# Kernel tuning notes

Hardware: AMD Instinct MI355X
Metric: run time of the kernel (lower is better)

## Reference

```python
import jax, jax.numpy as jnp
import numpy as np

# Layered-DAG regularization of the dynamic active_path graph.
H, N, BATCH, D, R = 6, 16, 32, 512, 64   # hop levels, nodes/level, batch, dim, low-rank
M = (H - 1) * N                           # nodes with weights (levels 1..H-1)
ETA_W = 0.015
LAM_C, LAM_R = 0.65, 0.35
THETA0 = 0.5
SPEC_MIN, SPEC_MAX = 0.3, 4.0
BETA1, BETA2, EPS = 0.9, 0.999, 1e-8
W_MAX = float(np.sqrt(D) * 2.0)
DW_CLIP = 5.0


def _spectral_norm(A1, B1):
    # largest singular value of W = A1 @ B1.T via power iteration using only low-rank products
    d = A1.shape[0]
    def body(_, u):
        w = A1 @ (B1.T @ (B1 @ (A1.T @ u)))  # (W W^T) u
        return w / (jnp.linalg.norm(w) + 1e-12)
    u0 = jnp.ones((d,), A1.dtype) / jnp.sqrt(jnp.asarray(d, A1.dtype))
    u = jax.lax.fori_loop(0, 20, body, u0)
    return jnp.linalg.norm(B1 @ (A1.T @ u))


def _update_node(A1, B1, mA, vA, mB, vB, Vin, T_local):
    # dual-signal (contrastive + retrograde) weight update, Adam step t=1, is_positive=True
    W = A1 @ B1.T                       # (D, D)
    Vw = Vin @ W.T                      # (BATCH, D) pre-activation (record.V_weighted)
    Vout = jnp.tanh(Vw)                 # record.V_out (tanh primitive)
    fprime = 1.0 - Vout ** 2            # primitive_derivative for tanh
    goodness = (Vout ** 2).sum(-1).mean()
    theta = THETA0 * ((Vin ** 2).sum(-1).mean() + 1e-9)   # goodness_scale_input=True
    delta = goodness - theta
    Vout_grad = (Vout * fprime * delta).mean(0)
    Vin_mean = Vin.mean(0)
    dW_c = jnp.outer(Vout_grad, Vin_mean)
    dW_r = jnp.outer(T_local.mean(0) * fprime.mean(0), Vin_mean)
    dW = LAM_C * dW_c + LAM_R * dW_r
    gnorm = jnp.linalg.norm(dW)
    dW = dW * jnp.where(gnorm > DW_CLIP, DW_CLIP / (gnorm + 1e-12), 1.0)
    gA = dW @ B1
    gB = dW.T @ A1
    mA_n = BETA1 * mA + (1 - BETA1) * gA
    vA_n = BETA2 * vA + (1 - BETA2) * gA ** 2
    A_new = A1 - ETA_W * (mA_n / (1 - BETA1)) / (jnp.sqrt(vA_n / (1 - BETA2)) + EPS)
    mB_n = BETA1 * mB + (1 - BETA1) * gB
    vB_n = BETA2 * vB + (1 - BETA2) * gB ** 2
    B_new = B1 - ETA_W * (mB_n / (1 - BETA1)) / (jnp.sqrt(vB_n / (1 - BETA2)) + EPS)
    return jnp.clip(A_new, -W_MAX, W_MAX), jnp.clip(B_new, -W_MAX, W_MAX)


def _forward(Y_hat, Y_star, V_edges, A, Bw, m_A, v_A, m_B, v_B):
    T_v = (Y_star - Y_hat) / jnp.sqrt(jnp.asarray(D, Y_hat.dtype))
    mse = jnp.mean((Y_star - Y_hat) ** 2)

    # proportional blame: per-edge mean-over-batch L2 norm of the contribution
    norms = jnp.linalg.norm(V_edges, axis=-1).mean(-1)           # (H-1, Ndst, Nsrc)
    w_blame = norms / (norms.sum(-1, keepdims=True) + 1e-9)

    spec = jax.vmap(jax.vmap(_spectral_norm))(A, Bw)             # (H-1, N)
    scale = jax.lax.stop_gradient(jnp.clip(spec, SPEC_MIN, SPEC_MAX))  # torch.tensor() detaches

    # retrograde flow in reverse topological (hop) order; output node = (level H-1, node 0)
    T_top = jnp.zeros((N, BATCH, D), Y_hat.dtype).at[0].set(T_v)

    def step(T_curr, xs):
        w_h, s_h = xs                                            # (Ndst,Nsrc), (Ndst,)
        tnorm = jnp.linalg.norm(T_curr, axis=-1).mean(-1)        # (Ndst,)
        edge_t = s_h[:, None] * w_h * tnorm[:, None]             # ||T_upstream|| per edge
        T_prev = jnp.einsum('j,ji,jbd->ibd', s_h, w_h, T_curr)   # blame-weighted scatter
        return T_prev, (T_prev, edge_t)

    _, (Ts, edge_t) = jax.lax.scan(step, T_top, (w_blame[::-1], scale[::-1]))
    T_all = jnp.concatenate([Ts[::-1], T_top[None]], axis=0)     # (H, N, BATCH, D), by level
    edge_tensions = edge_t[::-1]                                 # (H-1, Ndst, Nsrc)

    V_in = V_edges.sum(axis=2)                                   # inbox sum -> (H-1, N, BATCH, D)
    T_upd = T_all[1:]                                            # tensions at non-input nodes

    sh = (M, D, R)
    A_new, B_new = jax.vmap(_update_node)(
        A.reshape(sh), Bw.reshape(sh), m_A.reshape(sh), v_A.reshape(sh),
        m_B.reshape(sh), v_B.reshape(sh),
        V_in.reshape(M, BATCH, D), T_upd.reshape(M, BATCH, D))
    return (mse, edge_tensions,
            A_new.reshape(H - 1, N, D, R), B_new.reshape(H - 1, N, D, R), T_all)


def setup_inputs():
    key = jax.random.key(0)
    k = jax.random.split(key, 7)
    sd = 1.0 / np.sqrt(D)
    return {
        "Y_hat": jax.random.normal(k[0], (BATCH, D), jnp.float32),
        "Y_star": jax.random.normal(k[1], (BATCH, D), jnp.float32),
        "V_edges": jax.random.normal(k[2], (H - 1, N, N, BATCH, D), jnp.float32),
        "A": jax.random.normal(k[3], (H - 1, N, D, R), jnp.float32) * sd,
        "Bw": jax.random.normal(k[4], (H - 1, N, D, R), jnp.float32) * sd,
        "m_A": jnp.zeros((H - 1, N, D, R), jnp.float32),
        "v_A": jax.random.uniform(k[5], (H - 1, N, D, R), jnp.float32) * 1e-4,
        "m_B": jnp.zeros((H - 1, N, D, R), jnp.float32),
        "v_B": jax.random.uniform(k[6], (H - 1, N, D, R), jnp.float32) * 1e-4,
    }


def reference(Y_hat, Y_star, V_edges, A, Bw, m_A, v_A, m_B, v_B):
    return _forward(Y_hat, Y_star, V_edges, A, Bw, m_A, v_A, m_B, v_B)
```

## Files before the change

### kernel.cpp

```cpp
#include <hip/hip_runtime.h>
#include <math.h>

#define DEV static __device__ __forceinline__

constexpr int NB    = 16;
constexpr int BATCH = 32;
constexpr int DDIM  = 512;
constexpr int RK    = 64;
constexpr int LAY   = 5;
constexpr int MM    = 80;
constexpr int TLS   = NB * BATCH * DDIM;

constexpr float ETA_W   = 0.015f;
constexpr float LAM_C   = 0.65f, LAM_R = 0.35f;
constexpr float THETA0  = 0.5f;
constexpr float SPEC_MIN = 0.3f, SPEC_MAX = 4.0f;
constexpr float DW_CLIP = 5.0f;
constexpr float W_MAX   = 45.254833995939045f;
constexpr float RSQ_D   = 0.044194173824159216f;

constexpr int OUT_MSE  = 0;
constexpr int OUT_EDGE = 1;
constexpr int OUT_A    = 1281;
constexpr int OUT_B    = OUT_A + MM * DDIM * RK;
constexpr int OUT_T    = OUT_B + MM * DDIM * RK;

constexpr int SCR_GP   = 1284;
constexpr int SCR_VIN  = SCR_GP + 2621440;

constexpr int WS_NORMB  = 0;
constexpr int WS_TVN    = 40960;
constexpr int WS_TVM    = 41000;
constexpr int WS_COEF   = 41600;
constexpr int WS_SCALE  = 41700;
constexpr int WS_Y0P    = 41800;
constexpr int WS_VM     = 62300;
constexpr int WS_P      = 103300;
constexpr int WS_Q      = 108450;
constexpr int WS_GC     = 113600;

DEV float wave_reduce(float v) {
  #pragma unroll
  for (int o = 32; o > 0; o >>= 1) v += __shfl_down(v, o, 64);
  return v;
}

DEV float block_reduce_512(float v, float* sred) {
  v = wave_reduce(v);
  __syncthreads();
  if ((threadIdx.x & 63) == 0) sred[threadIdx.x >> 6] = v;
  __syncthreads();
  float s = 0.f;
  #pragma unroll
  for (int k = 0; k < 8; ++k) s += sred[k];
  return s;
}

DEV float bcast_lane(float v, int lane) {
  return __int_as_float(__builtin_amdgcn_readlane(__float_as_int(v), lane));
}

__global__ __launch_bounds__(256) void k_stage1(const float* __restrict__ V,
    const float* __restrict__ yh, const float* __restrict__ ys,
    const float* __restrict__ Aw, const float* __restrict__ Bww,
    float* __restrict__ out, float* __restrict__ ws) {
  __shared__ float smem[8448];
  int bid = blockIdx.x, t = threadIdx.x;
  if (bid < 2560) {
    float* nbuf = smem;
    float* vbuf = smem + 2048;
    int b = bid & 31, j = (bid >> 5) & 15, hh = bid >> 9;
    const float* base = V + (size_t)(((hh*16 + j)*16)*32 + b) * 512;
    int g = t >> 7, u = t & 127;
    float vx = 0.f, vy = 0.f, vz = 0.f, vw = 0.f;
    #pragma unroll
    for (int io = 0; io < 8; ++io) {
      int i = io * 2 + g;
      float4 v = ((const float4*)(base + (size_t)i * 16384))[u];
      nbuf[i * 128 + u] = v.x*v.x + v.y*v.y + v.z*v.z + v.w*v.w;
      vx += v.x; vy += v.y; vz += v.z; vw += v.w;
    }
    vbuf[g * 512 + u * 4 + 0] = vx;
    vbuf[g * 512 + u * 4 + 1] = vy;
    vbuf[g * 512 + u * 4 + 2] = vz;
    vbuf[g * 512 + u * 4 + 3] = vw;
    __syncthreads();
    {
      float2 o;
      o.x = vbuf[2 * t]     + vbuf[512 + 2 * t];
      o.y = vbuf[2 * t + 1] + vbuf[512 + 2 * t + 1];
      ((float2*)(out + SCR_VIN + (size_t)((hh*16 + j)*32 + b) * 512))[t] = o;
    }
    int w = t >> 6, lane = t & 63;
    #pragma unroll
    for (int k = 0; k < 4; ++k) {
      int i = w * 4 + k;
      float s = nbuf[i * 128 + lane] + nbuf[i * 128 + lane + 64];
      s = wave_reduce(s);
      if (lane == 0)
        ws[WS_NORMB + (size_t)b * 1280 + (hh*16 + j) * 16 + i] = sqrtf(s);
    }
  } else if (bid < 2592) {
    int b = bid - 2560;
    float2 a = ((const float2*)(yh + (size_t)b * 512))[t];
    float2 c = ((const float2*)(ys + (size_t)b * 512))[t];
    float d0 = c.x - a.x, d1 = c.y - a.y;
    float s = d0*d0 + d1*d1;
    s = wave_reduce(s);
    if ((t & 63) == 0) smem[t >> 6] = s;
    __syncthreads();
    if (t == 0)
      ws[WS_TVN + b] = sqrtf(smem[0]+smem[1]+smem[2]+smem[3]) * RSQ_D;
  } else if (bid == 2592) {
    float s = 0.f;
    for (int i = t; i < 4096; i += 256) {
      float4 a = ((const float4*)yh)[i], b = ((const float4*)ys)[i];
      float d0 = b.x-a.x, d1 = b.y-a.y, d2 = b.z-a.z, d3 = b.w-a.w;
      s += d0*d0 + d1*d1 + d2*d2 + d3*d3;
    }
    s = wave_reduce(s);
    if ((t & 63) == 0) smem[t >> 6] = s;
    __syncthreads();
    if (t == 0)
      out[OUT_MSE] = (smem[0]+smem[1]+smem[2]+smem[3]) * (1.f/16384.f);
  } else if (bid == 2593) {
    float s0 = 0.f, s1 = 0.f;
    #pragma unroll 4
    for (int b = 0; b < 32; ++b) {
      s0 += ys[b*512 + t]       - yh[b*512 + t];
      s1 += ys[b*512 + t + 256] - yh[b*512 + t + 256];
    }
    ws[WS_TVM + t]       = s0 * (RSQ_D / 32.f);
    ws[WS_TVM + t + 256] = s1 * (RSQ_D / 32.f);
  } else {
    float* tile = smem;
    float (*y0s)[64] = (float(*)[64])(smem + 8192);
    int bid0 = bid - 2594;
    int slice = bid0 & 3, side = (bid0 >> 2) & 1, m = bid0 >> 3;
    const float* src = (side ? Bww : Aw) + (size_t)m * 32768 + slice * 8192;
    #pragma unroll
    for (int k = 0; k < 8; ++k)
      ((float4*)tile)[t + k * 256] = ((const float4*)src)[t + k * 256];
    __syncthreads();
    {
      int r = t & 63, q = t >> 6;
      float s = 0.f;
      #pragma unroll 8
      for (int dd = q * 32; dd < q * 32 + 32; ++dd) s += tile[dd * 64 + r];
      y0s[q][r] = s;
    }
    __syncthreads();
    if (side == 0 && t < 64)
      ws[WS_Y0P + (m * 4 + slice) * 64 + t] = y0s[0][t] + y0s[1][t] + y0s[2][t] + y0s[3][t];
    float acc[4][4];
    #pragma unroll
    for (int i = 0; i < 4; ++i)
      #pragma unroll
      for (int k = 0; k < 4; ++k) acc[i][k] = 0.f;
    int r1 = (t >> 4) * 4, r2 = (t & 15) * 4;
    #pragma unroll 4
    for (int dd = 0; dd < 128; ++dd) {
      float4 a1 = *(const float4*)&tile[dd * 64 + r1];
      float4 a2 = *(const float4*)&tile[dd * 64 + r2];
      float av[4] = {a1.x, a1.y, a1.z, a1.w};
      float bv[4] = {a2.x, a2.y, a2.z, a2.w};
      #pragma unroll
      for (int i = 0; i < 4; ++i)
        #pragma unroll
        for (int k = 0; k < 4; ++k) acc[i][k] += av[i] * bv[k];
    }
    float* outp = out + SCR_GP + (size_t)((m * 2 + side) * 4 + slice) * 4096;
    #pragma unroll
    for (int i = 0; i < 4; ++i) {
      float4 v; v.x = acc[i][0]; v.y = acc[i][1]; v.z = acc[i][2]; v.w = acc[i][3];
      *(float4*)&outp[(r1 + i) * 64 + r2] = v;
    }
  }
}

__global__ __launch_bounds__(64, 1) void k_power(const float* __restrict__ out,
                                                 float* __restrict__ ws) {
  int m = blockIdx.x;
  int r = threadIdx.x;
  const float* gp = out + SCR_GP + (size_t)(m * 2 + 0) * 16384;
  const float* hp = out + SCR_GP + (size_t)(m * 2 + 1) * 16384;
  float Gc[64], Hc[64];
  #pragma unroll
  for (int c4 = 0; c4 < 16; ++c4) {
    const float* gb = gp + r * 64 + c4 * 4;
    float4 g0 = *(const float4*)(gb);
    float4 g1 = *(const float4*)(gb + 4096);
    float4 g2 = *(const float4*)(gb + 8192);
    float4 g3 = *(const float4*)(gb + 12288);
    Gc[c4*4+0] = g0.x+g1.x+g2.x+g3.x;
    Gc[c4*4+1] = g0.y+g1.y+g2.y+g3.y;
    Gc[c4*4+2] = g0.z+g1.z+g2.z+g3.z;
    Gc[c4*4+3] = g0.w+g1.w+g2.w+g3.w;
    const float* hb = hp + r * 64 + c4 * 4;
    float4 h0 = *(const float4*)(hb);
    float4 h1 = *(const float4*)(hb + 4096);
    float4 h2 = *(const float4*)(hb + 8192);
    float4 h3 = *(const float4*)(hb + 12288);
    Hc[c4*4+0] = h0.x+h1.x+h2.x+h3.x;
    Hc[c4*4+1] = h0.y+h1.y+h2.y+h3.y;
    Hc[c4*4+2] = h0.z+h1.z+h2.z+h3.z;
    Hc[c4*4+3] = h0.w+h1.w+h2.w+h3.w;
  }
  float y = (ws[WS_Y0P + (m*4+0)*64 + r] + ws[WS_Y0P + (m*4+1)*64 + r] +
             ws[WS_Y0P + (m*4+2)*64 + r] + ws[WS_Y0P + (m*4+3)*64 + r]) * RSQ_D;
  for (int it = 0; it < 20; ++it) {
    float z0 = 0.f, z1 = 0.f, z2 = 0.f, z3 = 0.f;
    #pragma unroll
    for (int c = 0; c < 16; ++c) {
      z0 = fmaf(Hc[c],      bcast_lane(y, c),      z0);
      z1 = fmaf(Hc[c + 16], bcast_lane(y, c + 16), z1);
      z2 = fmaf(Hc[c + 32], bcast_lane(y, c + 32), z2);
      z3 = fmaf(Hc[c + 48], bcast_lane(y, c + 48), z3);
    }
    float z = (z0 + z1) + (z2 + z3);
    float t0 = 0.f, t1 = 0.f, t2 = 0.f, t3 = 0.f;
    #pragma unroll
    for (int c = 0; c < 16; ++c) {
      t0 = fmaf(Gc[c],      bcast_lane(z, c),      t0);
      t1 = fmaf(Gc[c + 16], bcast_lane(z, c + 16), t1);
      t2 = fmaf(Gc[c + 32], bcast_lane(z, c + 32), t2);
      t3 = fmaf(Gc[c + 48], bcast_lane(z, c + 48), t3);
    }
    float tt = (t0 + t1) + (t2 + t3);
    float zt = z * tt;
    #pragma unroll
    for (int o = 32; o > 0; o >>= 1) zt += __shfl_xor(zt, o, 64);
    y = tt / (sqrtf(zt) + 1e-12f);
  }
  float z0 = 0.f, z1 = 0.f, z2 = 0.f, z3 = 0.f;
  #pragma unroll
  for (int c = 0; c < 16; ++c) {
    z0 = fmaf(Hc[c],      bcast_lane(y, c),      z0);
    z1 = fmaf(Hc[c + 16], bcast_lane(y, c + 16), z1);
    z2 = fmaf(Hc[c + 32], bcast_lane(y, c + 32), z2);
    z3 = fmaf(Hc[c + 48], bcast_lane(y, c + 48), z3);
  }
  float z = (z0 + z1) + (z2 + z3);
  float yz = y * z;
  #pragma unroll
  for (int o = 32; o > 0; o >>= 1) yz += __shfl_xor(yz, o, 64);
  if (r == 0)
    ws[WS_SCALE + m] = fminf(fmaxf(sqrtf(yz), SPEC_MIN), SPEC_MAX);
}

constexpr int MTP = 516;
constexpr int YVP = 36;

__global__ __launch_bounds__(512) void k_node(const float* __restrict__ Aw,
    const float* __restrict__ Bww, float* __restrict__ out, float* __restrict__ ws) {
  __shared__ float MT[64 * MTP];
  __shared__ float R2[4096];
  __shared__ float gcol[512];
  __shared__ float sred[8];
  __shared__ float coefs[96];
  int m = blockIdx.x;
  int t = threadIdx.x;
  const float* A1  = Aw  + (size_t)m * 32768;
  const float* B1  = Bww + (size_t)m * 32768;
  const float* Vin = out + SCR_VIN + (size_t)m * 16384;
  int hh = m >> 4, j = m & 15;

  if (t < 256) {
    #pragma unroll
    for (int h = 0; h < 5; ++h) {
      float n = 0.f;
      #pragma unroll 8
      for (int b = 0; b < 32; ++b)
        n += ws[WS_NORMB + (size_t)b * 1280 + h * 256 + t];
      n *= (1.f / 32.f);
      float s = n;
      s += __shfl_xor(s, 1, 64);
      s += __shfl_xor(s, 2, 64);
      s += __shfl_xor(s, 4, 64);
      s += __shfl_xor(s, 8, 64);
      R2[h * 256 + t] = ws[WS_SCALE + h * 16 + (t >> 4)] * n / (s + 1e-9f);
    }
    if (t < 16) coefs[80 + t] = (t == 0) ? 1.f : 0.f;
  }
  __syncthreads();
  if (t < 16) {
    for (int h = 4; h >= 0; --h) {
      float s = 0.f;
      #pragma unroll
      for (int jj = 0; jj < 16; ++jj)
        s += R2[h * 256 + jj * 16 + t] * coefs[(h + 1) * 16 + jj];
      coefs[h * 16 + t] = s;
    }
  }
  __syncthreads();
  if (m == 0) {
    if (t < 256) {
      float tvs = 0.f;
      #pragma unroll
      for (int b = 0; b < 32; ++b) tvs += ws[WS_TVN + b];
      float tvmean = tvs * (1.f / 32.f);
      #pragma unroll
      for (int h = 0; h < 5; ++h)
        out[OUT_EDGE + h * 256 + t] = R2[h * 256 + t] * coefs[(h + 1) * 16 + (t >> 4)] * tvmean;
    }
    if (t < 96) ws[WS_COEF + t] = coefs[t];
  }
  float coefval = coefs[(hh + 1) * 16 + j];

  auto stageT = [&](const float* src) {
    #pragma unroll
    for (int ch = 0; ch < 16; ++ch) {
      int g = ch * 2048 + t * 4;
      int d = g >> 6, r = g & 63;
      float4 v = *(const float4*)(src + g);
      MT[(r+0)*MTP + d] = v.x;
      MT[(r+1)*MTP + d] = v.y;
      MT[(r+2)*MTP + d] = v.z;
      MT[(r+3)*MTP + d] = v.w;
    }
  };

  stageT(B1);
  __syncthreads();

  {
    int rl = t & 31, bq = t >> 5;
    int b0 = bq * 2;
    float a00 = 0.f, a01 = 0.f, a10 = 0.f, a11 = 0.f;
    const float4* vp0 = (const float4*)(Vin + (size_t)b0 * 512);
    const float4* vp1 = (const float4*)(Vin + (size_t)(b0 + 1) * 512);
    #pragma unroll 4
    for (int d4 = 0; d4 < 128; ++d4) {
      float4 m0 = *(const float4*)&MT[rl * MTP + d4 * 4];
      float4 m1 = *(const float4*)&MT[(rl + 32) * MTP + d4 * 4];
      float4 v0 = vp0[d4];
      float4 v1 = vp1[d4];
      a00 += m0.x*v0.x + m0.y*v0.y + m0.z*v0.z + m0.w*v0.w;
      a01 += m0.x*v1.x + m0.y*v1.y + m0.z*v1.z + m0.w*v1.w;
      a10 += m1.x*v0.x + m1.y*v0.y + m1.z*v0.z + m1.w*v0.w;
      a11 += m1.x*v1.x + m1.y*v1.y + m1.z*v1.z + m1.w*v1.w;
    }
    R2[rl * YVP + b0]            = a00;
    R2[rl * YVP + b0 + 1]        = a01;
    R2[(rl + 32) * YVP + b0]     = a10;
    R2[(rl + 32) * YVP + b0 + 1] = a11;
  }
  __syncthreads();
  if (t < 64) {
    float s = 0.f;
    #pragma unroll 8
    for (int b = 0; b < 32; ++b) s += R2[t * YVP + b];
    ws[WS_P + m * 64 + t] = s * (1.f / 32.f);
  }
  float tmean, ssin, ssvm;
  {
    int d = t;
    float sv = 0.f, sq = 0.f;
    #pragma unroll 4
    for (int b = 0; b < 32; ++b) {
      float v = Vin[b * 512 + d];
      sv += v; sq += v * v;
    }
    float vmean = sv * (1.f / 32.f);
    tmean = coefval * ws[WS_TVM + d];
    ws[WS_VM + m * 512 + d] = vmean;
    ssin = block_reduce_512(sq, sred) * (1.f / 32.f);
    ssvm = block_reduce_512(vmean * vmean, sred);
  }
  __syncthreads();
  stageT(A1);
  __syncthreads();
  float gs = 0.f;
  float vga[4] = {0.f, 0.f, 0.f, 0.f}, fpa[4] = {0.f, 0.f, 0.f, 0.f};
  {
    int d4 = t >> 2, bg = t & 3;
    float acc[4][8];
    #pragma unroll
    for (int i = 0; i < 4; ++i)
      #pragma unroll
      for (int k = 0; k < 8; ++k) acc[i][k] = 0.f;
    #pragma unroll 2
    for (int rr = 0; rr < 64; ++rr) {
      float4 at = *(const float4*)&MT[rr * MTP + d4 * 4];
      float4 ya = *(const float4*)&R2[rr * YVP + bg * 8];
      float4 yb = *(const float4*)&R2[rr * YVP + bg * 8 + 4];
      float av[4] = {at.x, at.y, at.z, at.w};
      float yv[8] = {ya.x, ya.y, ya.z, ya.w, yb.x, yb.y, yb.z, yb.w};
      #pragma unroll
      for (int i = 0; i < 4; ++i)
        #pragma unroll
        for (int k = 0; k < 8; ++k) acc[i][k] += av[i] * yv[k];
    }
    #pragma unroll
    for (int i = 0; i < 4; ++i)
      #pragma unroll
      for (int k = 0; k < 8; ++k) {
        float vw = acc[i][k];
        float x = fminf(fmaxf(vw * 2.f, -40.f), 40.f);
        float e = __expf(x);
        float vo = (e - 1.f) / (e + 1.f);
        float fp = 1.f - vo * vo;
        gs += vo * vo;
        vga[i] += vo * fp;
        fpa[i] += fp;
      }
  }
  __syncthreads();
  {
    int d4 = t >> 2, bg = t & 3;
    #pragma unroll
    for (int i = 0; i < 4; ++i) {
      R2[bg * 512 + d4 * 4 + i] = vga[i];
      R2[2048 + bg * 512 + d4 * 4 + i] = fpa[i];
    }
  }
  float goodness = block_reduce_512(gs, sred) * (1.f / 32.f);
  float delta = goodness - THETA0 * (ssin + 1e-9f);
  {
    int d = t;
    float vg = R2[d] + R2[512 + d] + R2[1024 + d] + R2[1536 + d];
    float fp = R2[2048 + d] + R2[2048 + 512 + d] + R2[2048 + 1024 + d] + R2[2048 + 1536 + d];
    float g = LAM_C * delta * vg * (1.f / 32.f) + LAM_R * tmean * (fp * (1.f / 32.f));
    float gn2 = block_reduce_512(g * g, sred);
    float gnorm = sqrtf(gn2) * sqrtf(ssvm);
    float clipf = gnorm > DW_CLIP ? DW_CLIP / (gnorm + 1e-12f) : 1.f;
    float gcv = g * clipf;
    ws[WS_GC + m * 512 + d] = gcv;
    gcol[d] = gcv;
  }
  __syncthreads();
  {
    int r = t & 63, dq = t >> 6;
    float s = 0.f;
    #pragma unroll
    for (int k = 0; k < 16; ++k) {
      int d = dq * 64 + k * 4;
      float4 at = *(const float4*)&MT[r * MTP + d];
      float4 gv = *(const float4*)&gcol[d];
      s += at.x*gv.x + at.y*gv.y + at.z*gv.z + at.w*gv.w;
    }
    R2[dq * 64 + r] = s;
  }
  __syncthreads();
  if (t < 64) {
    float s = 0.f;
    #pragma unroll
    for (int p8 = 0; p8 < 8; ++p8) s += R2[p8 * 64 + t];
    ws[WS_Q + m * 64 + t] = s;
  }
}

constexpr int TW_BLOCKS = 1536;
constexpr int AD_HALF4  = 655360;

__global__ __launch_bounds__(256) void k_final(const float* __restrict__ yh,
    const float* __restrict__ ys,
    const float* __restrict__ Aw, const float* __restrict__ Bww,
    const float* __restrict__ mA, const float* __restrict__ vA,
    const float* __restrict__ mB, const float* __restrict__ vB,
    const float* __restrict__ ws, float* __restrict__ out) {
  int bid = blockIdx.x, t = threadIdx.x;
  if (bid < TW_BLOCKS) {
    int g0 = (bid * 256 + t) * 4;
    int li = g0 >> 14;
    int bd = g0 & 16383;
    float4 a = *(const float4*)(yh + bd);
    float4 b = *(const float4*)(ys + bd);
    float cf = ws[WS_COEF + li] * RSQ_D;
    out[OUT_T + g0 + 0] = cf * (b.x - a.x);
    out[OUT_T + g0 + 1] = cf * (b.y - a.y);
    out[OUT_T + g0 + 2] = cf * (b.z - a.z);
    out[OUT_T + g0 + 3] = cf * (b.w - a.w);
    return;
  }
  int idx = (bid - TW_BLOCKS) * 256 + t;
  bool isB = idx >= AD_HALF4;
  int e = (isB ? idx - AD_HALF4 : idx) * 4;
  int m = e >> 15;
  int rem = e & 32767;
  int d = rem >> 6;
  int r = rem & 63;
  float4 g4;
  const float *w0, *m0, *v0;
  int obase;
  if (!isB) {
    float gc = ws[WS_GC + m * 512 + d];
    float4 p = *(const float4*)&ws[WS_P + m * 64 + r];
    g4.x = gc * p.x; g4.y = gc * p.y; g4.z = gc * p.z; g4.w = gc * p.w;
    w0 = Aw; m0 = mA; v0 = vA; obase = OUT_A;
  } else {
    float vm = ws[WS_VM + m * 512 + d];
    float4 q = *(const float4*)&ws[WS_Q + m * 64 + r];
    g4.x = vm * q.x; g4.y = vm * q.y; g4.z = vm * q.z; g4.w = vm * q.w;
    w0 = Bww; m0 = mB; v0 = vB; obase = OUT_B;
  }
  float4 a4 = *(const float4*)&w0[e];
  float4 mm4 = *(const float4*)&m0[e];
  float4 vv4 = *(const float4*)&v0[e];
  float ga[4] = {g4.x, g4.y, g4.z, g4.w};
  float aa[4] = {a4.x, a4.y, a4.z, a4.w};
  float ma[4] = {mm4.x, mm4.y, mm4.z, mm4.w};
  float va[4] = {vv4.x, vv4.y, vv4.z, vv4.w};
  #pragma unroll
  for (int i = 0; i < 4; ++i) {
    float g = ga[i];
    float mn = 0.9f * ma[i] + 0.1f * g;
    float vn = 0.999f * va[i] + 0.001f * g * g;
    float u = aa[i] - ETA_W * (mn * 10.f) / (sqrtf(vn * 1000.f) + 1e-8f);
    u = fminf(fmaxf(u, -W_MAX), W_MAX);
    out[obase + e + i] = u;
  }
}

extern "C" void kernel_launch(void* const* d_in, const int* in_sizes, int n_in,
                              void* d_out, int out_size, void* d_ws, size_t ws_size,
                              hipStream_t stream) {
  (void)in_sizes; (void)n_in; (void)out_size; (void)ws_size;
  const float* Yh = (const float*)d_in[0];
  const float* Ys = (const float*)d_in[1];
  const float* V  = (const float*)d_in[2];
  const float* Aw = (const float*)d_in[3];
  const float* Bw = (const float*)d_in[4];
  const float* mA = (const float*)d_in[5];
  const float* vA = (const float*)d_in[6];
  const float* mB = (const float*)d_in[7];
  const float* vB = (const float*)d_in[8];
  float* out = (float*)d_out;
  float* ws  = (float*)d_ws;

  k_stage1<<<2594 + 640, 256, 0, stream>>>(V, Yh, Ys, Aw, Bw, out, ws);
  k_power<<<80, 64, 0, stream>>>(out, ws);
  k_node<<<80, 512, 0, stream>>>(Aw, Bw, out, ws);
  k_final<<<TW_BLOCKS + 2 * (AD_HALF4 / 256), 256, 0, stream>>>(
      Yh, Ys, Aw, Bw, mA, vA, mB, vB, ws, out);
}
```

Baseline: 116.3 us.

## Split per-node kernel into Yv GEMV kernel and Vw kernel using pre-transposed A

Moves the B^T·Vin product out of the 80-block node kernel into a separate 160-block kernel, and has stage1 write a transposed copy of A into scratch so the node kernel reads A^T from global memory instead of staging it transposed in a large LDS buffer. The stage1 tile is padded to reduce bank conflicts. The intent is to cut the large per-block LDS footprint and the serial staging work in the low-occupancy node kernel. In exchange it adds a kernel launch, extra global writes and reads of the transposed A, and uncached global reads inside the inner GEMM loop.

```diff
diff --git a/kernel.cpp b/kernel.cpp
--- a/kernel.cpp
+++ b/kernel.cpp
@@ -26,7 +26,9 @@
 constexpr int OUT_T    = OUT_B + MM * DDIM * RK;
 
 constexpr int SCR_GP   = 1284;
-constexpr int SCR_VIN  = SCR_GP + 2621440;
+constexpr int SCR_YV   = 1284;
+constexpr int SCR_AT   = 2622724;
+constexpr int SCR_VIN  = 5244164;
 
 constexpr int WS_NORMB  = 0;
 constexpr int WS_TVN    = 40960;
@@ -60,11 +62,13 @@
   return __int_as_float(__builtin_amdgcn_readlane(__float_as_int(v), lane));
 }
 
+constexpr int GTP = 68;
+
 __global__ __launch_bounds__(256) void k_stage1(const float* __restrict__ V,
     const float* __restrict__ yh, const float* __restrict__ ys,
     const float* __restrict__ Aw, const float* __restrict__ Bww,
     float* __restrict__ out, float* __restrict__ ws) {
-  __shared__ float smem[8448];
+  __shared__ float smem[128 * GTP + 256];
   int bid = blockIdx.x, t = threadIdx.x;
   if (bid < 2560) {
     float* nbuf = smem;
@@ -134,24 +138,40 @@
     ws[WS_TVM + t + 256] = s1 * (RSQ_D / 32.f);
   } else {
     float* tile = smem;
-    float (*y0s)[64] = (float(*)[64])(smem + 8192);
+    float (*y0s)[64] = (float(*)[64])(smem + 128 * GTP);
     int bid0 = bid - 2594;
     int slice = bid0 & 3, side = (bid0 >> 2) & 1, m = bid0 >> 3;
     const float* src = (side ? Bww : Aw) + (size_t)m * 32768 + slice * 8192;
     #pragma unroll
-    for (int k = 0; k < 8; ++k)
-      ((float4*)tile)[t + k * 256] = ((const float4*)src)[t + k * 256];
+    for (int k = 0; k < 8; ++k) {
+      int g = (t + k * 256) * 4;
+      int dd = g >> 6, r = g & 63;
+      *(float4*)&tile[dd * GTP + r] = ((const float4*)src)[t + k * 256];
+    }
     __syncthreads();
     {
       int r = t & 63, q = t >> 6;
       float s = 0.f;
       #pragma unroll 8
-      for (int dd = q * 32; dd < q * 32 + 32; ++dd) s += tile[dd * 64 + r];
+      for (int dd = q * 32; dd < q * 32 + 32; ++dd) s += tile[dd * GTP + r];
       y0s[q][r] = s;
     }
     __syncthreads();
-    if (side == 0 && t < 64)
-      ws[WS_Y0P + (m * 4 + slice) * 64 + t] = y0s[0][t] + y0s[1][t] + y0s[2][t] + y0s[3][t];
+    if (side == 0) {
+      if (t < 64)
+        ws[WS_Y0P + (m * 4 + slice) * 64 + t] = y0s[0][t] + y0s[1][t] + y0s[2][t] + y0s[3][t];
+      int dd0 = t & 31, rg = t >> 5;
+      #pragma unroll
+      for (int rb = 0; rb < 8; ++rb) {
+        int r = rb * 8 + rg;
+        float4 v;
+        v.x = tile[(dd0*4 + 0) * GTP + r];
+        v.y = tile[(dd0*4 + 1) * GTP + r];
+        v.z = tile[(dd0*4 + 2) * GTP + r];
+        v.w = tile[(dd0*4 + 3) * GTP + r];
+        *(float4*)&out[SCR_AT + (size_t)m * 32768 + r * 512 + slice * 128 + dd0 * 4] = v;
+      }
+    }
     float acc[4][4];
     #pragma unroll
     for (int i = 0; i < 4; ++i)
@@ -160,8 +180,8 @@
     int r1 = (t >> 4) * 4, r2 = (t & 15) * 4;
     #pragma unroll 4
     for (int dd = 0; dd < 128; ++dd) {
-      float4 a1 = *(const float4*)&tile[dd * 64 + r1];
-      float4 a2 = *(const float4*)&tile[dd * 64 + r2];
+      float4 a1 = *(const float4*)&tile[dd * GTP + r1];
+      float4 a2 = *(const float4*)&tile[dd * GTP + r2];
       float av[4] = {a1.x, a1.y, a1.z, a1.w};
       float bv[4] = {a2.x, a2.y, a2.z, a2.w};
       #pragma unroll
@@ -248,22 +268,54 @@
     ws[WS_SCALE + m] = fminf(fmaxf(sqrtf(yz), SPEC_MIN), SPEC_MAX);
 }
 
-constexpr int MTP = 516;
+__global__ __launch_bounds__(256) void k_yv(const float* __restrict__ Bww,
+                                            float* __restrict__ out) {
+  int bid = blockIdx.x;
+  int m = bid >> 1, half = bid & 1;
+  int t = threadIdx.x;
+  int w = t >> 6, r = t & 63;
+  int b0 = half * 16 + w * 4;
+  const float* Bm  = Bww + (size_t)m * 32768;
+  const float* Vm  = out + SCR_VIN + (size_t)m * 16384;
+  float acc0 = 0.f, acc1 = 0.f, acc2 = 0.f, acc3 = 0.f;
+  #pragma unroll 2
+  for (int d = 0; d < 512; d += 4) {
+    float br0 = Bm[(d+0)*64 + r];
+    float br1 = Bm[(d+1)*64 + r];
+    float br2 = Bm[(d+2)*64 + r];
+    float br3 = Bm[(d+3)*64 + r];
+    float4 v0 = *(const float4*)(Vm + (b0+0)*512 + d);
+    float4 v1 = *(const float4*)(Vm + (b0+1)*512 + d);
+    float4 v2 = *(const float4*)(Vm + (b0+2)*512 + d);
+    float4 v3 = *(const float4*)(Vm + (b0+3)*512 + d);
+    acc0 += br0*v0.x + br1*v0.y + br2*v0.z + br3*v0.w;
+    acc1 += br0*v1.x + br1*v1.y + br2*v1.z + br3*v1.w;
+    acc2 += br0*v2.x + br1*v2.y + br2*v2.z + br3*v2.w;
+    acc3 += br0*v3.x + br1*v3.y + br2*v3.z + br3*v3.w;
+  }
+  float* Yv = out + SCR_YV + (size_t)m * 2048;
+  Yv[(b0+0)*64 + r] = acc0;
+  Yv[(b0+1)*64 + r] = acc1;
+  Yv[(b0+2)*64 + r] = acc2;
+  Yv[(b0+3)*64 + r] = acc3;
+}
+
 constexpr int YVP = 36;
 
-__global__ __launch_bounds__(512) void k_node(const float* __restrict__ Aw,
-    const float* __restrict__ Bww, float* __restrict__ out, float* __restrict__ ws) {
-  __shared__ float MT[64 * MTP];
-  __shared__ float R2[4096];
+__global__ __launch_bounds__(512) void k_vw(const float* __restrict__ Aw,
+    float* __restrict__ out, float* __restrict__ ws) {
+  __shared__ float YvT[64 * YVP];
+  __shared__ float comb[4096];
   __shared__ float gcol[512];
   __shared__ float sred[8];
   __shared__ float coefs[96];
   int m = blockIdx.x;
   int t = threadIdx.x;
+  int hh = m >> 4, j = m & 15;
   const float* A1  = Aw  + (size_t)m * 32768;
-  const float* B1  = Bww + (size_t)m * 32768;
+  const float* ATm = out + SCR_AT  + (size_t)m * 32768;
   const float* Vin = out + SCR_VIN + (size_t)m * 16384;
-  int hh = m >> 4, j = m & 15;
+  const float* YvG = out + SCR_YV  + (size_t)m * 2048;
 
   if (t < 256) {
     #pragma unroll
@@ -278,7 +330,7 @@
       s += __shfl_xor(s, 2, 64);
       s += __shfl_xor(s, 4, 64);
       s += __shfl_xor(s, 8, 64);
-      R2[h * 256 + t] = ws[WS_SCALE + h * 16 + (t >> 4)] * n / (s + 1e-9f);
+      comb[h * 256 + t] = ws[WS_SCALE + h * 16 + (t >> 4)] * n / (s + 1e-9f);
     }
     if (t < 16) coefs[80 + t] = (t == 0) ? 1.f : 0.f;
   }
@@ -288,7 +340,7 @@
       float s = 0.f;
       #pragma unroll
       for (int jj = 0; jj < 16; ++jj)
-        s += R2[h * 256 + jj * 16 + t] * coefs[(h + 1) * 16 + jj];
+        s += comb[h * 256 + jj * 16 + t] * coefs[(h + 1) * 16 + jj];
       coefs[h * 16 + t] = s;
     }
   }
@@ -301,55 +353,26 @@
       float tvmean = tvs * (1.f / 32.f);
       #pragma unroll
       for (int h = 0; h < 5; ++h)
-        out[OUT_EDGE + h * 256 + t] = R2[h * 256 + t] * coefs[(h + 1) * 16 + (t >> 4)] * tvmean;
+        out[OUT_EDGE + h * 256 + t] = comb[h * 256 + t] * coefs[(h + 1) * 16 + (t >> 4)] * tvmean;
     }
     if (t < 96) ws[WS_COEF + t] = coefs[t];
   }
   float coefval = coefs[(hh + 1) * 16 + j];
-
-  auto stageT = [&](const float* src) {
-    #pragma unroll
-    for (int ch = 0; ch < 16; ++ch) {
-      int g = ch * 2048 + t * 4;
-      int d = g >> 6, r = g & 63;
-      float4 v = *(const float4*)(src + g);
-      MT[(r+0)*MTP + d] = v.x;
-      MT[(r+1)*MTP + d] = v.y;
-      MT[(r+2)*MTP + d] = v.z;
-      MT[(r+3)*MTP + d] = v.w;
-    }
-  };
-
-  stageT(B1);
   __syncthreads();
 
   {
-    int rl = t & 31, bq = t >> 5;
-    int b0 = bq * 2;
-    float a00 = 0.f, a01 = 0.f, a10 = 0.f, a11 = 0.f;
-    const float4* vp0 = (const float4*)(Vin + (size_t)b0 * 512);
-    const float4* vp1 = (const float4*)(Vin + (size_t)(b0 + 1) * 512);
-    #pragma unroll 4
-    for (int d4 = 0; d4 < 128; ++d4) {
-      float4 m0 = *(const float4*)&MT[rl * MTP + d4 * 4];
-      float4 m1 = *(const float4*)&MT[(rl + 32) * MTP + d4 * 4];
-      float4 v0 = vp0[d4];
-      float4 v1 = vp1[d4];
-      a00 += m0.x*v0.x + m0.y*v0.y + m0.z*v0.z + m0.w*v0.w;
-      a01 += m0.x*v1.x + m0.y*v1.y + m0.z*v1.z + m0.w*v1.w;
-      a10 += m1.x*v0.x + m1.y*v0.y + m1.z*v0.z + m1.w*v0.w;
-      a11 += m1.x*v1.x + m1.y*v1.y + m1.z*v1.z + m1.w*v1.w;
-    }
-    R2[rl * YVP + b0]            = a00;
-    R2[rl * YVP + b0 + 1]        = a01;
-    R2[(rl + 32) * YVP + b0]     = a10;
-    R2[(rl + 32) * YVP + b0 + 1] = a11;
+    int b = t >> 4, rq = t & 15;
+    float4 y4 = *(const float4*)(YvG + b * 64 + rq * 4);
+    YvT[(rq*4 + 0) * YVP + b] = y4.x;
+    YvT[(rq*4 + 1) * YVP + b] = y4.y;
+    YvT[(rq*4 + 2) * YVP + b] = y4.z;
+    YvT[(rq*4 + 3) * YVP + b] = y4.w;
   }
   __syncthreads();
   if (t < 64) {
     float s = 0.f;
     #pragma unroll 8
-    for (int b = 0; b < 32; ++b) s += R2[t * YVP + b];
+    for (int b = 0; b < 32; ++b) s += YvT[t * YVP + b];
     ws[WS_P + m * 64 + t] = s * (1.f / 32.f);
   }
   float tmean, ssin, ssvm;
@@ -367,9 +390,6 @@
     ssin = block_reduce_512(sq, sred) * (1.f / 32.f);
     ssvm = block_reduce_512(vmean * vmean, sred);
   }
-  __syncthreads();
-  stageT(A1);
-  __syncthreads();
   float gs = 0.f;
   float vga[4] = {0.f, 0.f, 0.f, 0.f}, fpa[4] = {0.f, 0.f, 0.f, 0.f};
   {
@@ -381,9 +401,9 @@
       for (int k = 0; k < 8; ++k) acc[i][k] = 0.f;
     #pragma unroll 2
     for (int rr = 0; rr < 64; ++rr) {
-      float4 at = *(const float4*)&MT[rr * MTP + d4 * 4];
-      float4 ya = *(const float4*)&R2[rr * YVP + bg * 8];
-      float4 yb = *(const float4*)&R2[rr * YVP + bg * 8 + 4];
+      float4 at = *(const float4*)(ATm + rr * 512 + d4 * 4);
+      float4 ya = *(const float4*)&YvT[rr * YVP + bg * 8];
+      float4 yb = *(const float4*)&YvT[rr * YVP + bg * 8 + 4];
       float av[4] = {at.x, at.y, at.z, at.w};
       float yv[8] = {ya.x, ya.y, ya.z, ya.w, yb.x, yb.y, yb.z, yb.w};
       #pragma unroll
@@ -395,8 +415,8 @@
     for (int i = 0; i < 4; ++i)
       #pragma unroll
       for (int k = 0; k < 8; ++k) {
-        float vw = acc[i][k];
-        float x = fminf(fmaxf(vw * 2.f, -40.f), 40.f);
+        float vwv = acc[i][k];
+        float x = fminf(fmaxf(vwv * 2.f, -40.f), 40.f);
         float e = __expf(x);
         float vo = (e - 1.f) / (e + 1.f);
         float fp = 1.f - vo * vo;
@@ -410,16 +430,16 @@
     int d4 = t >> 2, bg = t & 3;
     #pragma unroll
     for (int i = 0; i < 4; ++i) {
-      R2[bg * 512 + d4 * 4 + i] = vga[i];
-      R2[2048 + bg * 512 + d4 * 4 + i] = fpa[i];
+      comb[bg * 512 + d4 * 4 + i] = vga[i];
+      comb[2048 + bg * 512 + d4 * 4 + i] = fpa[i];
     }
   }
   float goodness = block_reduce_512(gs, sred) * (1.f / 32.f);
   float delta = goodness - THETA0 * (ssin + 1e-9f);
   {
     int d = t;
-    float vg = R2[d] + R2[512 + d] + R2[1024 + d] + R2[1536 + d];
-    float fp = R2[2048 + d] + R2[2048 + 512 + d] + R2[2048 + 1024 + d] + R2[2048 + 1536 + d];
+    float vg = comb[d] + comb[512 + d] + comb[1024 + d] + comb[1536 + d];
+    float fp = comb[2048 + d] + comb[2048 + 512 + d] + comb[2048 + 1024 + d] + comb[2048 + 1536 + d];
     float g = LAM_C * delta * vg * (1.f / 32.f) + LAM_R * tmean * (fp * (1.f / 32.f));
     float gn2 = block_reduce_512(g * g, sred);
     float gnorm = sqrtf(gn2) * sqrtf(ssvm);
@@ -432,20 +452,18 @@
   {
     int r = t & 63, dq = t >> 6;
     float s = 0.f;
-    #pragma unroll
-    for (int k = 0; k < 16; ++k) {
-      int d = dq * 64 + k * 4;
-      float4 at = *(const float4*)&MT[r * MTP + d];
-      float4 gv = *(const float4*)&gcol[d];
-      s += at.x*gv.x + at.y*gv.y + at.z*gv.z + at.w*gv.w;
-    }
-    R2[dq * 64 + r] = s;
+    #pragma unroll 4
+    for (int k = 0; k < 64; ++k) {
+      int d = dq * 64 + k;
+      s += gcol[d] * A1[d * 64 + r];
+    }
+    comb[dq * 64 + r] = s;
   }
   __syncthreads();
   if (t < 64) {
     float s = 0.f;
     #pragma unroll
-    for (int p8 = 0; p8 < 8; ++p8) s += R2[p8 * 64 + t];
+    for (int p8 = 0; p8 < 8; ++p8) s += comb[p8 * 64 + t];
     ws[WS_Q + m * 64 + t] = s;
   }
 }
@@ -530,7 +548,8 @@
 
   k_stage1<<<2594 + 640, 256, 0, stream>>>(V, Yh, Ys, Aw, Bw, out, ws);
   k_power<<<80, 64, 0, stream>>>(out, ws);
-  k_node<<<80, 512, 0, stream>>>(Aw, Bw, out, ws);
+  k_yv<<<160, 256, 0, stream>>>(Bw, out);
+  k_vw<<<80, 512, 0, stream>>>(Aw, out, ws);
   k_final<<<TW_BLOCKS + 2 * (AD_HALF4 / 256), 256, 0, stream>>>(
       Yh, Ys, Aw, Bw, mA, vA, mB, vB, ws, out);
 }
```

Measured after the change: 140.3 us. +20.6%, slower.
